# Optimization experiments

Hardware: AMD Instinct MI355X
Metric: run time of the kernel (lower is better)

## Reference

```python
import jax, jax.numpy as jnp
import numpy as np

NEG = -1000.0   # mask value used by reduce_func for zero scores
SLOPE = 0.01    # default F.leaky_relu negative slope
N_NODES, N_EDGES, D_IN, D_OUT, N_HEADS = 100000, 1600000, 256, 64, 4


def setup_inputs() -> dict:
    key = jax.random.key(0)
    k0, k1, k2, k3, k4 = jax.random.split(key, 5)
    h = jax.random.normal(k0, (N_NODES, D_IN), jnp.float32)
    src = jax.random.randint(k1, (N_EDGES,), 0, N_NODES)
    dst = jax.random.randint(k2, (N_EDGES,), 0, N_NODES)
    # per-head fc weight [H, Din, Dout] and attn_fc weight [H, 2*Dout]
    W = jax.random.normal(k3, (N_HEADS, D_IN, D_OUT), jnp.float32) / np.sqrt(D_IN)
    att = jax.random.normal(k4, (N_HEADS, 2 * D_OUT), jnp.float32) / np.sqrt(2.0 * D_OUT)
    return {"h": h, "W": W, "att": att, "src": src, "dst": dst}


def reference(h, W, att, src, dst):
    N = h.shape[0]
    H, _, F = W.shape
    # per-head linear projection (dropout is identity in eval mode)
    z = jnp.einsum('nd,hdf->nhf', h, W)                      # [N,H,F]
    # leaky_relu([z_src||z_dst] @ a) == leaky_relu(z_src@a1 + z_dst@a2)
    a_src, a_dst = att[:, :F], att[:, F:]
    es = jnp.einsum('nhf,hf->nh', z, a_src)                  # [N,H]
    ed = jnp.einsum('nhf,hf->nh', z, a_dst)                  # [N,H]
    e = jax.nn.leaky_relu(es[src] + ed[dst], SLOPE)          # [E,H]
    # reduce_func replaces exact-zero scores with -1000 before softmax
    e = jnp.where(e == 0.0, NEG, e)
    # segment (per-destination) softmax, numerically stable
    m = jax.ops.segment_max(e, dst, num_segments=N)          # [N,H]
    m = jnp.where(jnp.isfinite(m), m, 0.0)                   # empty segments
    ex = jnp.exp(e - m[dst])                                 # [E,H]
    denom = jax.ops.segment_sum(ex, dst, num_segments=N)     # [N,H]
    safe = jnp.where(denom[dst] > 0.0, denom[dst], 1.0)
    alpha = ex / safe                                        # [E,H]
    # weighted scatter-sum of source features to destinations
    out = jax.ops.segment_sum(alpha[:, :, None] * z[src], dst, num_segments=N)  # [N,H,F]
    # merge='cat' over heads
    return out.reshape(N, H * F)
```

## Files before the change

kernel.cpp:

```cpp
#include <hip/hip_runtime.h>
#include <math.h>

#define NEGV (-1000.0f)
#define SLOPE 0.01f
#define D_IN 256
#define LDK 72

typedef _Float16 half8 __attribute__((ext_vector_type(8)));
typedef _Float16 half4h __attribute__((ext_vector_type(4)));
typedef float f32x4 __attribute__((ext_vector_type(4)));

__device__ __forceinline__ int rli(int v, int l) {
    return __builtin_amdgcn_readlane(v, l);
}
__device__ __forceinline__ void nt_store2(float* p, float a, float b) {
    float2 v = make_float2(a, b);
    __builtin_nontemporal_store(__builtin_bit_cast(double, v), (double*)p);
}

__global__ void wprep_kernel(const float* __restrict__ W, _Float16* __restrict__ Wt_hi,
                             _Float16* __restrict__ Wt_lo) {
    int i = blockIdx.x * 256 + threadIdx.x;
    int f = i & 63;
    int k = (i >> 6) & 255;
    int h = i >> 14;
    float w = W[i];
    _Float16 hi = (_Float16)w;
    _Float16 lo = (_Float16)(w - (float)hi);
    int c = f * 4 + h;
    Wt_hi[c * 256 + k] = hi;
    Wt_lo[c * 256 + k] = lo;
}

__global__ __launch_bounds__(512) void gemm_kernel(const float* __restrict__ hmat,
        const _Float16* __restrict__ Wt_hi, const _Float16* __restrict__ Wt_lo,
        float* __restrict__ z_t, int N) {
    __shared__ __align__(16) _Float16 smem[4 * 128 * LDK];
    _Float16* A_hi = smem;
    _Float16* A_lo = smem + 128 * LDK;
    _Float16* B_hi = smem + 2 * 128 * LDK;
    _Float16* B_lo = smem + 3 * 128 * LDK;
    const int t = threadIdx.x;
    const int lane = t & 63;
    const int w = t >> 6;
    const int quad = lane >> 4;
    const int m16 = lane & 15;
    const int rg = w & 3;
    const int cg = w >> 2;
    const int n0 = (blockIdx.x >> 1) * 128;
    const int c0 = (blockIdx.x & 1) * 128;

    f32x4 acc[2][4];
#pragma unroll
    for (int rt = 0; rt < 2; rt++)
#pragma unroll
        for (int ct = 0; ct < 4; ct++) acc[rt][ct] = (f32x4){0.f, 0.f, 0.f, 0.f};

    for (int kc = 0; kc < 256; kc += 64) {
        __syncthreads();
#pragma unroll
        for (int i = 0; i < 4; i++) {
            int idx = i * 512 + t;
            int row = idx >> 4, q = idx & 15;
            int rr = min(n0 + row, N - 1);
            float4 v = *(const float4*)&hmat[(size_t)rr * 256 + kc + q * 4];
            half4h hv, lv;
            hv[0] = (_Float16)v.x; lv[0] = (_Float16)(v.x - (float)hv[0]);
            hv[1] = (_Float16)v.y; lv[1] = (_Float16)(v.y - (float)hv[1]);
            hv[2] = (_Float16)v.z; lv[2] = (_Float16)(v.z - (float)hv[2]);
            hv[3] = (_Float16)v.w; lv[3] = (_Float16)(v.w - (float)hv[3]);
            *(half4h*)&A_hi[row * LDK + q * 4] = hv;
            *(half4h*)&A_lo[row * LDK + q * 4] = lv;
        }
#pragma unroll
        for (int i = 0; i < 2; i++) {
            int idx = i * 512 + t;
            int c = idx >> 3, seg = idx & 7;
            float4 vh = *(const float4*)&Wt_hi[(c0 + c) * 256 + kc + seg * 8];
            float4 vl = *(const float4*)&Wt_lo[(c0 + c) * 256 + kc + seg * 8];
            *(float4*)&B_hi[c * LDK + seg * 8] = vh;
            *(float4*)&B_lo[c * LDK + seg * 8] = vl;
        }
        __syncthreads();
#pragma unroll
        for (int ks = 0; ks < 2; ks++) {
            half8 ah[2], al[2], bh[4], bl[4];
#pragma unroll
            for (int rt = 0; rt < 2; rt++) {
                int ro = ((rg * 2 + rt) * 16 + m16) * LDK + ks * 32 + quad * 8;
                ah[rt] = *(const half8*)&A_hi[ro];
                al[rt] = *(const half8*)&A_lo[ro];
            }
#pragma unroll
            for (int ct = 0; ct < 4; ct++) {
                int co = ((cg * 4 + ct) * 16 + m16) * LDK + ks * 32 + quad * 8;
                bh[ct] = *(const half8*)&B_hi[co];
                bl[ct] = *(const half8*)&B_lo[co];
            }
#pragma unroll
            for (int rt = 0; rt < 2; rt++)
#pragma unroll
                for (int ct = 0; ct < 4; ct++) {
                    acc[rt][ct] = __builtin_amdgcn_mfma_f32_16x16x32_f16(ah[rt], bh[ct], acc[rt][ct], 0, 0, 0);
                    acc[rt][ct] = __builtin_amdgcn_mfma_f32_16x16x32_f16(al[rt], bh[ct], acc[rt][ct], 0, 0, 0);
                    acc[rt][ct] = __builtin_amdgcn_mfma_f32_16x16x32_f16(ah[rt], bl[ct], acc[rt][ct], 0, 0, 0);
                }
        }
    }
#pragma unroll
    for (int rt = 0; rt < 2; rt++)
#pragma unroll
        for (int ct = 0; ct < 4; ct++)
#pragma unroll
            for (int r = 0; r < 4; r++) {
                int n = n0 + rg * 32 + rt * 16 + quad * 4 + r;
                int c = c0 + cg * 64 + ct * 16 + m16;
                if (n < N) z_t[(size_t)n * 256 + c] = acc[rt][ct][r];
            }
}

__global__ void esed_kernel(float* __restrict__ z_t, const float* __restrict__ att,
                            float* __restrict__ es_ed, int N) {
    int gid = blockIdx.x * blockDim.x + threadIdx.x;
    int n = gid >> 6;
    int lane = gid & 63;
    if (n >= N) return;
    float4 zv = *(const float4*)&z_t[(size_t)n * 256 + lane * 4];
    float ps0 = zv.x * att[0 * 128 + lane];
    float ps1 = zv.y * att[1 * 128 + lane];
    float ps2 = zv.z * att[2 * 128 + lane];
    float ps3 = zv.w * att[3 * 128 + lane];
    float pd0 = zv.x * att[0 * 128 + 64 + lane];
    float pd1 = zv.y * att[1 * 128 + 64 + lane];
    float pd2 = zv.z * att[2 * 128 + 64 + lane];
    float pd3 = zv.w * att[3 * 128 + 64 + lane];
    for (int off = 1; off < 64; off <<= 1) {
        ps0 += __shfl_xor(ps0, off); ps1 += __shfl_xor(ps1, off);
        ps2 += __shfl_xor(ps2, off); ps3 += __shfl_xor(ps3, off);
        pd0 += __shfl_xor(pd0, off); pd1 += __shfl_xor(pd1, off);
        pd2 += __shfl_xor(pd2, off); pd3 += __shfl_xor(pd3, off);
    }
    half4h h16;
    h16[0] = (_Float16)zv.x; h16[1] = (_Float16)zv.y;
    h16[2] = (_Float16)zv.z; h16[3] = (_Float16)zv.w;
    *(half4h*)((_Float16*)z_t + (size_t)n * 512 + 256 + lane * 4) = h16;
    if (lane == 0) {
        *(float4*)&es_ed[(size_t)n * 8]     = make_float4(ps0, ps1, ps2, ps3);
        *(float4*)&es_ed[(size_t)n * 8 + 4] = make_float4(pd0, pd1, pd2, pd3);
    }
}

__global__ void hist_kernel(const int* __restrict__ dst, int* __restrict__ counts,
                            int* __restrict__ slot, int E) {
    int i = blockIdx.x * blockDim.x + threadIdx.x;
    if (i < E) {
        int sl = atomicAdd(&counts[dst[i]], 1);
        slot[((i >> 7) << 8) + (i & 127)] = sl;
    }
}

__global__ void scanA_kernel(const int* __restrict__ counts, int* __restrict__ bsums, int N) {
    __shared__ int lds[256];
    int t = threadIdx.x;
    int base = blockIdx.x * 1024 + t * 4;
    int s = 0;
    if (base + 3 < N) {
        int4 v = *(const int4*)&counts[base];
        s = v.x + v.y + v.z + v.w;
    } else {
        for (int u = 0; u < 4; u++) if (base + u < N) s += counts[base + u];
    }
    lds[t] = s; __syncthreads();
    for (int off = 128; off > 0; off >>= 1) {
        if (t < off) lds[t] += lds[t + off];
        __syncthreads();
    }
    if (t == 0) bsums[blockIdx.x] = lds[0];
}

__global__ void scanB_kernel(int* __restrict__ bsums, int nb) {
    __shared__ int lds[256];
    int t = threadIdx.x;
    int v = (t < nb) ? bsums[t] : 0;
    lds[t] = v; __syncthreads();
    for (int off = 1; off < 256; off <<= 1) {
        int x = (t >= off) ? lds[t - off] : 0;
        __syncthreads();
        lds[t] += x;
        __syncthreads();
    }
    if (t < nb) bsums[t] = lds[t] - v;
}

__global__ void scanC_kernel(const int* __restrict__ counts, const int* __restrict__ bsums,
                             int* __restrict__ row_start, int N) {
    __shared__ int lds[256];
    int t = threadIdx.x;
    int base = blockIdx.x * 1024 + t * 4;
    int4 v = make_int4(0, 0, 0, 0);
    if (base + 3 < N) v = *(const int4*)&counts[base];
    else {
        if (base + 0 < N) v.x = counts[base + 0];
        if (base + 1 < N) v.y = counts[base + 1];
        if (base + 2 < N) v.z = counts[base + 2];
    }
    int s = v.x + v.y + v.z + v.w;
    lds[t] = s; __syncthreads();
    for (int off = 1; off < 256; off <<= 1) {
        int x = (t >= off) ? lds[t - off] : 0;
        __syncthreads();
        lds[t] += x;
        __syncthreads();
    }
    int excl = lds[t] - s + bsums[blockIdx.x];
    int4 r;
    r.x = excl; r.y = r.x + v.x; r.z = r.y + v.y; r.w = r.z + v.z;
    if (base + 3 < N) *(int4*)&row_start[base] = r;
    else {
        if (base + 0 < N) row_start[base + 0] = r.x;
        if (base + 1 < N) row_start[base + 1] = r.y;
        if (base + 2 < N) row_start[base + 2] = r.z;
    }
}

__global__ void scatter_kernel(const int* __restrict__ src, const int* __restrict__ dst,
                               const int* __restrict__ row_start, const int* __restrict__ slot,
                               int* __restrict__ csr_src, int E) {
    int i = blockIdx.x * blockDim.x + threadIdx.x;
    if (i < E) {
        int d = dst[i];
        csr_src[row_start[d] + slot[((i >> 7) << 8) + (i & 127)]] = src[i];
    }
}

__global__ __launch_bounds__(256) void aggregate_kernel(const _Float16* __restrict__ z16,
        const float* __restrict__ es_ed, const int* __restrict__ csr_src,
        const int* __restrict__ row_start, const int* __restrict__ counts,
        float* __restrict__ out, int N) {
    int gid = blockIdx.x * blockDim.x + threadIdx.x;
    int wv = gid >> 6;
    int lane = gid & 63;
    if (2 * wv >= N) return;
    int half = lane >> 5;
    int hl = lane & 31;
    int n = 2 * wv + half;
    int nn = min(n, N - 1);
    int cnt = counts[nn];
    int start = row_start[nn];
    float4 edn = *(const float4*)&es_ed[(size_t)nn * 8 + 4];
    int cmax = max(rli(cnt, 0), rli(cnt, 32));
    int hb = half << 5;

    float m0 = -INFINITY, m1 = -INFINITY, m2 = -INFINITY, m3 = -INFINITY;
    float l0 = 0.f, l1 = 0.f, l2 = 0.f, l3 = 0.f;
    float o0 = 0.f, o1 = 0.f, o2 = 0.f, o3 = 0.f;
    float o4 = 0.f, o5 = 0.f, o6 = 0.f, o7 = 0.f;

    for (int base = 0; base < cmax; base += 32) {
        int i = base + hl;
        int s = 0;
        float e0 = -INFINITY, e1 = -INFINITY, e2 = -INFINITY, e3 = -INFINITY;
        if (i < cnt) {
            s = csr_src[start + i];
            float4 esv = *(const float4*)&es_ed[(size_t)s * 8];
            float x0 = esv.x + edn.x; e0 = x0 > 0.f ? x0 : SLOPE * x0; if (e0 == 0.f) e0 = NEGV;
            float x1 = esv.y + edn.y; e1 = x1 > 0.f ? x1 : SLOPE * x1; if (e1 == 0.f) e1 = NEGV;
            float x2 = esv.z + edn.z; e2 = x2 > 0.f ? x2 : SLOPE * x2; if (e2 == 0.f) e2 = NEGV;
            float x3 = esv.w + edn.w; e3 = x3 > 0.f ? x3 : SLOPE * x3; if (e3 == 0.f) e3 = NEGV;
        }
        float c0 = e0, c1 = e1, c2 = e2, c3 = e3;
#pragma unroll
        for (int off = 1; off < 32; off <<= 1) {
            c0 = fmaxf(c0, __shfl_xor(c0, off)); c1 = fmaxf(c1, __shfl_xor(c1, off));
            c2 = fmaxf(c2, __shfl_xor(c2, off)); c3 = fmaxf(c3, __shfl_xor(c3, off));
        }
        float nm0 = fmaxf(m0, c0), nm1 = fmaxf(m1, c1), nm2 = fmaxf(m2, c2), nm3 = fmaxf(m3, c3);
        float sc0 = __expf(m0 - nm0), sc1 = __expf(m1 - nm1);
        float sc2 = __expf(m2 - nm2), sc3 = __expf(m3 - nm3);
        o0 *= sc0; o1 *= sc1; o2 *= sc2; o3 *= sc3;
        o4 *= sc0; o5 *= sc1; o6 *= sc2; o7 *= sc3;
        l0 *= sc0; l1 *= sc1; l2 *= sc2; l3 *= sc3;
        m0 = nm0; m1 = nm1; m2 = nm2; m3 = nm3;

        float p0 = 0.f, p1 = 0.f, p2 = 0.f, p3 = 0.f;
        if (i < cnt) {
            p0 = __expf(e0 - m0); p1 = __expf(e1 - m1);
            p2 = __expf(e2 - m2); p3 = __expf(e3 - m3);
        }
        l0 += p0; l1 += p1; l2 += p2; l3 += p3;

        int jmax = min(32, cmax - base);
        int j = 0;
        for (; j + 7 < jmax; j += 8) {
            half8 zz[8]; float4 qq[8];
#pragma unroll
            for (int u = 0; u < 8; u++) {
                int idx = hb + j + u;
                int ss = __shfl(s, idx);
                qq[u] = make_float4(__shfl(p0, idx), __shfl(p1, idx),
                                    __shfl(p2, idx), __shfl(p3, idx));
                zz[u] = *(const half8*)&z16[(size_t)ss * 512 + 256 + hl * 8];
            }
#pragma unroll
            for (int u = 0; u < 8; u++) {
                o0 += qq[u].x * (float)zz[u][0]; o1 += qq[u].y * (float)zz[u][1];
                o2 += qq[u].z * (float)zz[u][2]; o3 += qq[u].w * (float)zz[u][3];
                o4 += qq[u].x * (float)zz[u][4]; o5 += qq[u].y * (float)zz[u][5];
                o6 += qq[u].z * (float)zz[u][6]; o7 += qq[u].w * (float)zz[u][7];
            }
        }
        for (; j < jmax; ++j) {
            int idx = hb + j;
            int ss = __shfl(s, idx);
            float q0 = __shfl(p0, idx), q1 = __shfl(p1, idx);
            float q2 = __shfl(p2, idx), q3 = __shfl(p3, idx);
            half8 zv = *(const half8*)&z16[(size_t)ss * 512 + 256 + hl * 8];
            o0 += q0 * (float)zv[0]; o1 += q1 * (float)zv[1];
            o2 += q2 * (float)zv[2]; o3 += q3 * (float)zv[3];
            o4 += q0 * (float)zv[4]; o5 += q1 * (float)zv[5];
            o6 += q2 * (float)zv[6]; o7 += q3 * (float)zv[7];
        }
    }
#pragma unroll
    for (int off = 1; off < 32; off <<= 1) {
        l0 += __shfl_xor(l0, off); l1 += __shfl_xor(l1, off);
        l2 += __shfl_xor(l2, off); l3 += __shfl_xor(l3, off);
    }
    if (n < N) {
        if (cnt > 0) {
            o0 /= l0; o1 /= l1; o2 /= l2; o3 /= l3;
            o4 /= l0; o5 /= l1; o6 /= l2; o7 /= l3;
        }
        float* ob = &out[(size_t)n * 256 + 2 * hl];
        nt_store2(ob + 0,   o0, o4);
        nt_store2(ob + 64,  o1, o5);
        nt_store2(ob + 128, o2, o6);
        nt_store2(ob + 192, o3, o7);
    }
}

extern "C" void kernel_launch(void* const* d_in, const int* in_sizes, int n_in,
                              void* d_out, int out_size, void* d_ws, size_t ws_size,
                              hipStream_t stream) {
    const float* hmat = (const float*)d_in[0];
    const float* W    = (const float*)d_in[1];
    const float* att  = (const float*)d_in[2];
    const int*   src  = (const int*)d_in[3];
    const int*   dst  = (const int*)d_in[4];
    int N = in_sizes[0] / D_IN;
    int E = in_sizes[3];
    float* out = (float*)d_out;

    float* z_t      = (float*)d_ws;
    float* es_ed    = z_t + (size_t)N * 256;
    _Float16* Wt_hi = (_Float16*)(es_ed + (size_t)N * 8);
    _Float16* Wt_lo = Wt_hi + 65536;
    int*   counts   = (int*)(Wt_lo + 65536);
    int*   cursor   = counts + N;
    int*   row_start= cursor + N;
    int*   bsums    = row_start + N;
    int*   csr_src  = bsums + 256;
    int*   slot     = (int*)z_t;

    int NB = (N + 1023) / 1024;
    int aggBlocks = ((N + 1) / 2 + 3) / 4;

    hipMemsetAsync(counts, 0, (size_t)N * sizeof(int), stream);
    wprep_kernel<<<256, 256, 0, stream>>>(W, Wt_hi, Wt_lo);
    gemm_kernel<<<((N + 127) / 128) * 2, 512, 0, stream>>>(hmat, Wt_hi, Wt_lo, z_t, N);
    esed_kernel<<<(N * 64 + 255) / 256, 256, 0, stream>>>(z_t, att, es_ed, N);
    hist_kernel<<<(E + 255) / 256, 256, 0, stream>>>(dst, counts, slot, E);
    scanA_kernel<<<NB, 256, 0, stream>>>(counts, bsums, N);
    scanB_kernel<<<1, 256, 0, stream>>>(bsums, NB);
    scanC_kernel<<<NB, 256, 0, stream>>>(counts, bsums, row_start, N);
    scatter_kernel<<<(E + 255) / 256, 256, 0, stream>>>(src, dst, row_start, slot, csr_src, E);
    aggregate_kernel<<<aggBlocks, 256, 0, stream>>>((const _Float16*)z_t, es_ed, csr_src, row_start, counts, out, N);
}
```

Measured before the change: 513.3 us.

## Compute attention scores from h via folded W·a and store z directly as fp16

Precomputes W_h·a_src and W_h·a_dst vectors so per-node attention scores come from a GEMV on the input features instead of the projected z. The GEMM now writes z straight as fp16 into the layout the aggregation reads, which removes the fp32 z store and the separate esed read/convert pass. This trades that traffic for an extra streaming read of h. It also changes the rounding of the scores slightly, since they are now computed in fp32 from h rather than from z.

After: 527.9 us. 2.8% more time.

```diff
diff --git a/kernel.cpp b/kernel.cpp
--- a/kernel.cpp
+++ b/kernel.cpp
@@ -32,9 +32,20 @@
     Wt_lo[c * 256 + k] = lo;
 }
 
+__global__ void waprep_kernel(const float* __restrict__ W, const float* __restrict__ att,
+                              float* __restrict__ wa) {
+    int q = blockIdx.x;
+    int k = threadIdx.x;
+    int h = q & 3, sel = q >> 2;
+    float acc = 0.f;
+    for (int f = 0; f < 64; f++)
+        acc += W[((size_t)h * 256 + k) * 64 + f] * att[h * 128 + sel * 64 + f];
+    wa[q * 256 + k] = acc;
+}
+
 __global__ __launch_bounds__(512) void gemm_kernel(const float* __restrict__ hmat,
         const _Float16* __restrict__ Wt_hi, const _Float16* __restrict__ Wt_lo,
-        float* __restrict__ z_t, int N) {
+        _Float16* __restrict__ z16, int N) {
     __shared__ __align__(16) _Float16 smem[4 * 128 * LDK];
     _Float16* A_hi = smem;
     _Float16* A_lo = smem + 128 * LDK;
@@ -115,38 +126,43 @@
             for (int r = 0; r < 4; r++) {
                 int n = n0 + rg * 32 + rt * 16 + quad * 4 + r;
                 int c = c0 + cg * 64 + ct * 16 + m16;
-                if (n < N) z_t[(size_t)n * 256 + c] = acc[rt][ct][r];
-            }
-}
-
-__global__ void esed_kernel(float* __restrict__ z_t, const float* __restrict__ att,
-                            float* __restrict__ es_ed, int N) {
-    int gid = blockIdx.x * blockDim.x + threadIdx.x;
-    int n = gid >> 6;
-    int lane = gid & 63;
-    if (n >= N) return;
-    float4 zv = *(const float4*)&z_t[(size_t)n * 256 + lane * 4];
-    float ps0 = zv.x * att[0 * 128 + lane];
-    float ps1 = zv.y * att[1 * 128 + lane];
-    float ps2 = zv.z * att[2 * 128 + lane];
-    float ps3 = zv.w * att[3 * 128 + lane];
-    float pd0 = zv.x * att[0 * 128 + 64 + lane];
-    float pd1 = zv.y * att[1 * 128 + 64 + lane];
-    float pd2 = zv.z * att[2 * 128 + 64 + lane];
-    float pd3 = zv.w * att[3 * 128 + 64 + lane];
-    for (int off = 1; off < 64; off <<= 1) {
-        ps0 += __shfl_xor(ps0, off); ps1 += __shfl_xor(ps1, off);
-        ps2 += __shfl_xor(ps2, off); ps3 += __shfl_xor(ps3, off);
-        pd0 += __shfl_xor(pd0, off); pd1 += __shfl_xor(pd1, off);
-        pd2 += __shfl_xor(pd2, off); pd3 += __shfl_xor(pd3, off);
-    }
-    half4h h16;
-    h16[0] = (_Float16)zv.x; h16[1] = (_Float16)zv.y;
-    h16[2] = (_Float16)zv.z; h16[3] = (_Float16)zv.w;
-    *(half4h*)((_Float16*)z_t + (size_t)n * 512 + 256 + lane * 4) = h16;
-    if (lane == 0) {
-        *(float4*)&es_ed[(size_t)n * 8]     = make_float4(ps0, ps1, ps2, ps3);
-        *(float4*)&es_ed[(size_t)n * 8 + 4] = make_float4(pd0, pd1, pd2, pd3);
+                if (n < N) z16[(size_t)n * 512 + 256 + c] = (_Float16)acc[rt][ct][r];
+            }
+}
+
+__global__ __launch_bounds__(256) void esgemv_kernel(const float* __restrict__ hmat,
+        const float* __restrict__ wa, float* __restrict__ es_ed, int N) {
+    int lane = threadIdx.x & 63;
+    int wv0 = (blockIdx.x * blockDim.x + threadIdx.x) >> 6;
+    int nw = (gridDim.x * blockDim.x) >> 6;
+    float4 w0 = *(const float4*)&wa[0 * 256 + lane * 4];
+    float4 w1 = *(const float4*)&wa[1 * 256 + lane * 4];
+    float4 w2 = *(const float4*)&wa[2 * 256 + lane * 4];
+    float4 w3 = *(const float4*)&wa[3 * 256 + lane * 4];
+    float4 w4 = *(const float4*)&wa[4 * 256 + lane * 4];
+    float4 w5 = *(const float4*)&wa[5 * 256 + lane * 4];
+    float4 w6 = *(const float4*)&wa[6 * 256 + lane * 4];
+    float4 w7 = *(const float4*)&wa[7 * 256 + lane * 4];
+    for (int n = wv0; n < N; n += nw) {
+        float4 hv = *(const float4*)&hmat[(size_t)n * 256 + lane * 4];
+        float s0 = hv.x * w0.x + hv.y * w0.y + hv.z * w0.z + hv.w * w0.w;
+        float s1 = hv.x * w1.x + hv.y * w1.y + hv.z * w1.z + hv.w * w1.w;
+        float s2 = hv.x * w2.x + hv.y * w2.y + hv.z * w2.z + hv.w * w2.w;
+        float s3 = hv.x * w3.x + hv.y * w3.y + hv.z * w3.z + hv.w * w3.w;
+        float s4 = hv.x * w4.x + hv.y * w4.y + hv.z * w4.z + hv.w * w4.w;
+        float s5 = hv.x * w5.x + hv.y * w5.y + hv.z * w5.z + hv.w * w5.w;
+        float s6 = hv.x * w6.x + hv.y * w6.y + hv.z * w6.z + hv.w * w6.w;
+        float s7 = hv.x * w7.x + hv.y * w7.y + hv.z * w7.z + hv.w * w7.w;
+        for (int off = 1; off < 64; off <<= 1) {
+            s0 += __shfl_xor(s0, off); s1 += __shfl_xor(s1, off);
+            s2 += __shfl_xor(s2, off); s3 += __shfl_xor(s3, off);
+            s4 += __shfl_xor(s4, off); s5 += __shfl_xor(s5, off);
+            s6 += __shfl_xor(s6, off); s7 += __shfl_xor(s7, off);
+        }
+        if (lane == 0) {
+            *(float4*)&es_ed[(size_t)n * 8]     = make_float4(s0, s1, s2, s3);
+            *(float4*)&es_ed[(size_t)n * 8 + 4] = make_float4(s4, s5, s6, s7);
+        }
     }
 }
 
@@ -361,14 +377,16 @@
     int*   bsums    = row_start + N;
     int*   csr_src  = bsums + 256;
     int*   slot     = (int*)z_t;
+    float* wa       = (float*)cursor;
 
     int NB = (N + 1023) / 1024;
     int aggBlocks = ((N + 1) / 2 + 3) / 4;
 
     hipMemsetAsync(counts, 0, (size_t)N * sizeof(int), stream);
     wprep_kernel<<<256, 256, 0, stream>>>(W, Wt_hi, Wt_lo);
-    gemm_kernel<<<((N + 127) / 128) * 2, 512, 0, stream>>>(hmat, Wt_hi, Wt_lo, z_t, N);
-    esed_kernel<<<(N * 64 + 255) / 256, 256, 0, stream>>>(z_t, att, es_ed, N);
+    waprep_kernel<<<8, 256, 0, stream>>>(W, att, wa);
+    gemm_kernel<<<((N + 127) / 128) * 2, 512, 0, stream>>>(hmat, Wt_hi, Wt_lo, (_Float16*)z_t, N);
+    esgemv_kernel<<<2048, 256, 0, stream>>>(hmat, wa, es_ed, N);
     hist_kernel<<<(E + 255) / 256, 256, 0, stream>>>(dst, counts, slot, E);
     scanA_kernel<<<NB, 256, 0, stream>>>(counts, bsums, N);
     scanB_kernel<<<1, 256, 0, stream>>>(bsums, NB);
```
